# Performance work log

Measured on AMD Instinct MI355X. Metric: run time of the kernel, lower is better.

The kernel has to match this reference:

```python
import jax, jax.numpy as jnp
import numpy as np

B, C, D_MODEL, N_HEADS = 2, 2048, 1024, 16


def rotary_matrix(context_length: int, d: int) -> jnp.ndarray:
    """Faithful vectorization of get_rotary_matrix: theta = 10000^(-2*(i-1)/d)."""
    half = d // 2
    i = jnp.arange(half, dtype=jnp.float32)
    theta = 10000.0 ** (-2.0 * (i - 1.0) / d)          # note the (i-1), as in source
    m = jnp.arange(context_length, dtype=jnp.float32)
    ang = m[:, None] * theta                            # [C, d/2]
    c, s = jnp.cos(ang), jnp.sin(ang)
    ev = 2 * jnp.arange(half)
    od = ev + 1
    R = jnp.zeros((context_length, d, d), jnp.float32)
    R = R.at[:, ev, ev].set(c)
    R = R.at[:, ev, od].set(-s)
    R = R.at[:, od, ev].set(s)
    R = R.at[:, od, od].set(c)
    return R


def setup_inputs() -> dict:
    key = jax.random.key(0)
    k1, k2, k3, k4 = jax.random.split(key, 4)
    x = jax.random.normal(k1, (B, C, D_MODEL), dtype=jnp.float32)
    w_qkv = jax.random.normal(k2, (3 * D_MODEL, D_MODEL), dtype=jnp.float32) * 0.02
    w_out = jax.random.normal(k3, (D_MODEL, D_MODEL), dtype=jnp.float32) * 0.02
    b_out = jax.random.normal(k4, (D_MODEL,), dtype=jnp.float32) * 0.02
    return {"x": x, "w_qkv": w_qkv, "w_out": w_out, "b_out": b_out}


def reference(x, w_qkv, w_out, b_out):
    b, c, d = x.shape
    h = N_HEADS
    dh = d // h
    qkv = x @ w_qkv.T                                   # [B,C,3D]
    q, k, v = jnp.split(qkv, 3, axis=-1)
    # [B,C,D] -> [B,H,C,dh]
    q = q.reshape(b, c, h, dh).transpose(0, 2, 1, 3)
    k = k.reshape(b, c, h, dh).transpose(0, 2, 1, 3)
    v = v.reshape(b, c, h, dh).transpose(0, 2, 1, 3)
    R = rotary_matrix(c, dh)                            # [C,dh,dh]
    q_rot = jnp.einsum('bhci,cij->bhcj', q, R)
    k_rot = jnp.einsum('bhci,cij->bhcj', k, R)
    scale = jnp.sqrt(jnp.float32(dh))
    # exact math of the source: exp with no max subtraction, separate num/den
    attn_num = jnp.exp(jnp.einsum('bhqd,bhkd->bhqk', q_rot, k_rot) / scale)
    attn_den = jnp.exp(jnp.einsum('bhqd,bhkd->bhqk', q, k) / scale)
    attn_den = jnp.sum(attn_den, axis=-1, keepdims=True)
    attn = attn_num / attn_den
    causal = jnp.tril(jnp.ones((c, c), jnp.float32))[None, None]
    attn = jnp.where(causal == 0, 0.0, attn)
    y = jnp.einsum('bhqk,bhkd->bhqd', attn, v)
    y = y.transpose(0, 2, 1, 3).reshape(b, c, d)
    return y @ w_out.T + b_out
```

## Files before the change

kernel.cpp:

```cpp
#include <hip/hip_runtime.h>
#include <math.h>
#include <stdint.h>

#define BB 2
#define CC 2048
#define DD 1024
#define HH 16
#define DHH 64
#define HALF 32

typedef __attribute__((ext_vector_type(8))) short bf16x8;
typedef __attribute__((ext_vector_type(4))) float f32x4;
typedef unsigned int u32;

__device__ __forceinline__ ushort f2bf(float f) {
    uint32_t u = __builtin_bit_cast(uint32_t, f);
    u = (u + 0x7FFFu + ((u >> 16) & 1u)) >> 16;
    return (ushort)u;
}

__device__ __forceinline__ void gload16(const void* g, void* lds) {
    __builtin_amdgcn_global_load_lds(
        (const u32 __attribute__((address_space(1)))*)g,
        (u32 __attribute__((address_space(3)))*)lds, 16, 0, 0);
}

__global__ __launch_bounds__(256) void cast3_k(const float* __restrict__ x,
                                               const float* __restrict__ wq,
                                               const float* __restrict__ wo,
                                               ushort* __restrict__ xb,
                                               ushort* __restrict__ wqb,
                                               ushort* __restrict__ wob) {
    int id = blockIdx.x * 256 + threadIdx.x;
    const float* s;
    ushort* d;
    int off;
    if (id < 524288)       { s = x;  d = xb;  off = id; }
    else if (id < 917504)  { s = wq; d = wqb; off = id - 524288; }
    else                   { s = wo; d = wob; off = id - 917504; }
    float4 a = *reinterpret_cast<const float4*>(s + (size_t)off * 8);
    float4 b = *reinterpret_cast<const float4*>(s + (size_t)off * 8 + 4);
    bf16x8 o;
    o[0] = (short)f2bf(a.x); o[1] = (short)f2bf(a.y);
    o[2] = (short)f2bf(a.z); o[3] = (short)f2bf(a.w);
    o[4] = (short)f2bf(b.x); o[5] = (short)f2bf(b.y);
    o[6] = (short)f2bf(b.z); o[7] = (short)f2bf(b.w);
    *reinterpret_cast<bf16x8*>(d + (size_t)off * 8) = o;
}

__global__ __launch_bounds__(256) void rope_table_k(float* __restrict__ ct, float* __restrict__ st) {
    int idx = blockIdx.x * 256 + threadIdx.x;
    if (idx >= CC * HALF) return;
    int m = idx >> 5;
    int t = idx & 31;
    double theta_d = pow(10000.0, -2.0 * ((double)t - 1.0) / 64.0);
    float theta = (float)theta_d;
    float ang = (float)m * theta;
    ct[idx] = cosf(ang);
    st[idx] = sinf(ang);
}

__global__ __launch_bounds__(256) void qkv_gemm_mfma_k(const ushort* __restrict__ xb,
                                                       const ushort* __restrict__ wqb,
                                                       const float* __restrict__ ct,
                                                       const float* __restrict__ st,
                                                       ushort* __restrict__ q,
                                                       ushort* __restrict__ k,
                                                       ushort* __restrict__ qr,
                                                       ushort* __restrict__ kr,
                                                       ushort* __restrict__ vT3) {
    __shared__ ushort Al[128 * 64];
    __shared__ ushort Bl[128 * 64];
    const int tid = threadIdx.x;
    const int w = tid >> 6, l = tid & 63;
    const int l15 = l & 15, lg = l >> 4;
    const int wr = w >> 1, wc = w & 1;
    const int m0 = blockIdx.x * 128, n0 = blockIdx.y * 128;
    const int lrow = l >> 3, lch = l & 7;

    f32x4 acc[4][4];
#pragma unroll
    for (int i = 0; i < 4; i++)
#pragma unroll
        for (int j = 0; j < 4; j++) acc[i][j] = (f32x4){0.f, 0.f, 0.f, 0.f};

    for (int k0 = 0; k0 < 1024; k0 += 64) {
        __syncthreads();
#pragma unroll
        for (int c = 0; c < 4; c++) {
            int row = w * 32 + c * 8 + lrow;
            int gch = (lch ^ (row & 7)) * 8;
            gload16(xb + (size_t)(m0 + row) * 1024 + k0 + gch, &Al[(w * 32 + c * 8) * 64]);
            gload16(wqb + (size_t)(n0 + row) * 1024 + k0 + gch, &Bl[(w * 32 + c * 8) * 64]);
        }
        __syncthreads();
#pragma unroll
        for (int kk = 0; kk < 2; kk++) {
            bf16x8 a[4], b[4];
#pragma unroll
            for (int mt = 0; mt < 4; mt++) {
                int row = wr * 64 + mt * 16 + l15;
                a[mt] = *reinterpret_cast<const bf16x8*>(&Al[row * 64 + ((kk * 4 + lg) ^ (row & 7)) * 8]);
            }
#pragma unroll
            for (int nt = 0; nt < 4; nt++) {
                int row = wc * 64 + nt * 16 + l15;
                b[nt] = *reinterpret_cast<const bf16x8*>(&Bl[row * 64 + ((kk * 4 + lg) ^ (row & 7)) * 8]);
            }
#pragma unroll
            for (int mt = 0; mt < 4; mt++)
#pragma unroll
                for (int nt = 0; nt < 4; nt++)
                    acc[mt][nt] = __builtin_amdgcn_mfma_f32_16x16x32_bf16(a[mt], b[nt], acc[mt][nt], 0, 0, 0);
        }
    }
#pragma unroll
    for (int mt = 0; mt < 4; mt++)
#pragma unroll
        for (int nt = 0; nt < 4; nt++) {
            int n = n0 + wc * 64 + nt * 16 + l15;
            int part = n >> 10;
            int d = n & 1023;
            int h = d >> 6, dd = d & 63;
            int mbase = m0 + wr * 64 + mt * 16 + lg * 4;
            int bb = mbase >> 11, cpos = mbase & 2047;
            if (part == 2) {
                int kt = cpos >> 6, kcol = cpos & 63;
                ushort4 pk;
                pk.x = f2bf(acc[mt][nt][0]); pk.y = f2bf(acc[mt][nt][1]);
                pk.z = f2bf(acc[mt][nt][2]); pk.w = f2bf(acc[mt][nt][3]);
                size_t off = ((((size_t)(bb * HH + h)) * 32 + kt) * 64 + dd) * 64 + kcol;
                *reinterpret_cast<ushort4*>(vT3 + off) = pk;
            } else {
                ushort* dstu = (part == 0) ? q : k;
                ushort* dstr = (part == 0) ? qr : kr;
                const float sgn = (dd & 1) ? -1.f : 1.f;
                const int t = dd >> 1;
#pragma unroll
                for (int r = 0; r < 4; r++) {
                    float val = acc[mt][nt][r];
                    float par = __shfl_xor(val, 1, 64);
                    float c = ct[(cpos + r) * 32 + t];
                    float s = st[(cpos + r) * 32 + t];
                    float rot = val * c + sgn * par * s;
                    size_t base = (((size_t)bb * HH + h) * CC + (cpos + r)) * DHH + dd;
                    dstu[base] = f2bf(val);
                    dstr[base] = f2bf(rot);
                }
            }
        }
}

__global__ __launch_bounds__(256, 4) void attn_mfma_k(const ushort* __restrict__ qg,
                                                      const ushort* __restrict__ kg,
                                                      const ushort* __restrict__ vT3,
                                                      const ushort* __restrict__ qrg,
                                                      const ushort* __restrict__ krg,
                                                      ushort* __restrict__ y) {
    __shared__ ushort Kl[2][64 * 64];
    __shared__ ushort Krl[2][64 * 64];
    __shared__ ushort Pl[4][16 * 64];

    const int tid = threadIdx.x;
    const int w = tid >> 6, l = tid & 63;
    const int l15 = l & 15, lg = l >> 4;
    const int lrow = l >> 3, lch = l & 7;
    const int bid = blockIdx.x;
    const int bh = bid >> 5;
    const int xt = bid & 31;
    const int tile = (bid & 512) ? (31 - xt) : xt;
    const int q0 = tile * 64;
    const ushort* qb  = qg  + (size_t)bh * CC * DHH;
    const ushort* kb  = kg  + (size_t)bh * CC * DHH;
    const ushort* qrb = qrg + (size_t)bh * CC * DHH;
    const ushort* krb = krg + (size_t)bh * CC * DHH;
    const ushort* vtb = vT3 + (size_t)bh * 32 * 64 * 64;

    bf16x8 qf[2], qrf[2];
#pragma unroll
    for (int kk = 0; kk < 2; kk++) {
        int row = q0 + w * 16 + l15;
        qf[kk]  = *reinterpret_cast<const bf16x8*>(qb  + (size_t)row * DHH + kk * 32 + lg * 8);
        qrf[kk] = *reinterpret_cast<const bf16x8*>(qrb + (size_t)row * DHH + kk * 32 + lg * 8);
    }

    f32x4 yacc[4];
#pragma unroll
    for (int nt = 0; nt < 4; nt++) yacc[nt] = (f32x4){0.f, 0.f, 0.f, 0.f};
    float dacc = 0.f;

#define STAGE(KT, BUF)                                                                        \
    {                                                                                         \
        const int sk0 = (KT) * 64;                                                            \
        const bool sneed = ((KT) <= tile);                                                    \
        _Pragma("unroll")                                                                     \
        for (int c = 0; c < 2; c++) {                                                         \
            int row = w * 16 + c * 8 + lrow;                                                  \
            int gch = (lch ^ (row & 7)) * 8;                                                  \
            gload16(kb + (size_t)(sk0 + row) * DHH + gch, &Kl[BUF][(w * 16 + c * 8) * 64]);   \
            if (sneed)                                                                        \
                gload16(krb + (size_t)(sk0 + row) * DHH + gch, &Krl[BUF][(w * 16 + c * 8) * 64]); \
        }                                                                                     \
    }

    STAGE(0, 0);
    __syncthreads();
    int cur = 0;

    for (int kt = 0; kt < CC / 64; kt++) {
        const bool need = (kt <= tile);

        bf16x8 vf[4][2];
        if (need) {
            const ushort* vt0 = vtb + (size_t)kt * 64 * 64;
#pragma unroll
            for (int nt2 = 0; nt2 < 4; nt2++)
#pragma unroll
                for (int kk2 = 0; kk2 < 2; kk2++)
                    vf[nt2][kk2] = *reinterpret_cast<const bf16x8*>(
                        vt0 + (nt2 * 16 + l15) * 64 + kk2 * 32 + lg * 8);
        }

        if (kt + 1 < CC / 64) STAGE(kt + 1, cur ^ 1);

#pragma unroll
        for (int nt = 0; nt < 4; nt++) {
            f32x4 s = (f32x4){0.f, 0.f, 0.f, 0.f};
#pragma unroll
            for (int kk = 0; kk < 2; kk++) {
                int krow = nt * 16 + l15;
                bf16x8 ka = *reinterpret_cast<const bf16x8*>(
                    &Kl[cur][krow * 64 + ((kk * 4 + lg) ^ (krow & 7)) * 8]);
                s = __builtin_amdgcn_mfma_f32_16x16x32_bf16(ka, qf[kk], s, 0, 0, 0);
            }
#pragma unroll
            for (int r = 0; r < 4; r++)
                dacc += __builtin_amdgcn_exp2f(s[r] * 0.1803368801f);
        }

        if (need) {
            const bool diag = (kt == tile);
            const int qrow = q0 + w * 16 + l15;
#pragma unroll
            for (int nt = 0; nt < 4; nt++) {
                f32x4 s = (f32x4){0.f, 0.f, 0.f, 0.f};
#pragma unroll
                for (int kk = 0; kk < 2; kk++) {
                    int krow = nt * 16 + l15;
                    bf16x8 ka = *reinterpret_cast<const bf16x8*>(
                        &Krl[cur][krow * 64 + ((kk * 4 + lg) ^ (krow & 7)) * 8]);
                    s = __builtin_amdgcn_mfma_f32_16x16x32_bf16(ka, qrf[kk], s, 0, 0, 0);
                }
                float pe[4];
#pragma unroll
                for (int r = 0; r < 4; r++)
                    pe[r] = __builtin_amdgcn_exp2f(s[r] * 0.1803368801f);
                if (diag) {
#pragma unroll
                    for (int r = 0; r < 4; r++) {
                        int key = kt * 64 + nt * 16 + lg * 4 + r;
                        pe[r] = (key <= qrow) ? pe[r] : 0.f;
                    }
                }
                u32 pk0, pk1;
                asm("v_cvt_pk_bf16_f32 %0, %1, %2" : "=v"(pk0) : "v"(pe[0]), "v"(pe[1]));
                asm("v_cvt_pk_bf16_f32 %0, %1, %2" : "=v"(pk1) : "v"(pe[2]), "v"(pe[3]));
                int swzc = (nt * 2 + (lg >> 1)) ^ (l15 & 7);
                uint2 pr; pr.x = pk0; pr.y = pk1;
                *reinterpret_cast<uint2*>(&Pl[w][l15 * 64 + swzc * 8 + (lg & 1) * 4]) = pr;
            }
            bf16x8 pa[2];
#pragma unroll
            for (int kk2 = 0; kk2 < 2; kk2++) {
                int rc = (kk2 * 4 + lg) ^ (l15 & 7);
                pa[kk2] = *reinterpret_cast<const bf16x8*>(&Pl[w][l15 * 64 + rc * 8]);
            }
#pragma unroll
            for (int nt2 = 0; nt2 < 4; nt2++)
#pragma unroll
                for (int kk2 = 0; kk2 < 2; kk2++)
                    yacc[nt2] = __builtin_amdgcn_mfma_f32_16x16x32_bf16(pa[kk2], vf[nt2][kk2],
                                                                        yacc[nt2], 0, 0, 0);
        }
        __syncthreads();
        cur ^= 1;
    }

    float den = dacc;
    den += __shfl_xor(den, 16, 64);
    den += __shfl_xor(den, 32, 64);

    const int b = bh >> 4, h = bh & 15;
#pragma unroll
    for (int r = 0; r < 4; r++) {
        float dr = __shfl(den, lg * 4 + r, 64);
        float inv = 1.f / dr;
        int row = q0 + w * 16 + lg * 4 + r;
#pragma unroll
        for (int nt2 = 0; nt2 < 4; nt2++)
            y[((size_t)b * CC + row) * DD + h * DHH + nt2 * 16 + l15] = f2bf(yacc[nt2][r] * inv);
    }
#undef STAGE
}

__global__ __launch_bounds__(256) void out_proj_mfma_k(const ushort* __restrict__ yb,
                                                       const ushort* __restrict__ wob,
                                                       const float* __restrict__ bias,
                                                       float* __restrict__ out) {
    __shared__ ushort Al[128 * 64];
    __shared__ ushort Bl[128 * 64];
    const int tid = threadIdx.x;
    const int w = tid >> 6, l = tid & 63;
    const int l15 = l & 15, lg = l >> 4;
    const int wr = w >> 1, wc = w & 1;
    const int m0 = blockIdx.x * 128, n0 = blockIdx.y * 128;
    const int lrow = l >> 3, lch = l & 7;

    f32x4 acc[4][4];
#pragma unroll
    for (int i = 0; i < 4; i++)
#pragma unroll
        for (int j = 0; j < 4; j++) acc[i][j] = (f32x4){0.f, 0.f, 0.f, 0.f};

    for (int k0 = 0; k0 < 1024; k0 += 64) {
        __syncthreads();
#pragma unroll
        for (int c = 0; c < 4; c++) {
            int row = w * 32 + c * 8 + lrow;
            int gch = (lch ^ (row & 7)) * 8;
            gload16(yb + (size_t)(m0 + row) * 1024 + k0 + gch, &Al[(w * 32 + c * 8) * 64]);
            gload16(wob + (size_t)(n0 + row) * 1024 + k0 + gch, &Bl[(w * 32 + c * 8) * 64]);
        }
        __syncthreads();
#pragma unroll
        for (int kk = 0; kk < 2; kk++) {
            bf16x8 a[4], b[4];
#pragma unroll
            for (int mt = 0; mt < 4; mt++) {
                int row = wr * 64 + mt * 16 + l15;
                a[mt] = *reinterpret_cast<const bf16x8*>(&Al[row * 64 + ((kk * 4 + lg) ^ (row & 7)) * 8]);
            }
#pragma unroll
            for (int nt = 0; nt < 4; nt++) {
                int row = wc * 64 + nt * 16 + l15;
                b[nt] = *reinterpret_cast<const bf16x8*>(&Bl[row * 64 + ((kk * 4 + lg) ^ (row & 7)) * 8]);
            }
#pragma unroll
            for (int mt = 0; mt < 4; mt++)
#pragma unroll
                for (int nt = 0; nt < 4; nt++)
                    acc[mt][nt] = __builtin_amdgcn_mfma_f32_16x16x32_bf16(a[mt], b[nt], acc[mt][nt], 0, 0, 0);
        }
    }
#pragma unroll
    for (int mt = 0; mt < 4; mt++)
#pragma unroll
        for (int nt = 0; nt < 4; nt++) {
            int n = n0 + wc * 64 + nt * 16 + l15;
            float bv = bias[n];
#pragma unroll
            for (int r = 0; r < 4; r++) {
                int m = m0 + wr * 64 + mt * 16 + lg * 4 + r;
                out[(size_t)m * 1024 + n] = acc[mt][nt][r] + bv;
            }
        }
}

extern "C" void kernel_launch(void* const* d_in, const int* in_sizes, int n_in,
                              void* d_out, int out_size, void* d_ws, size_t ws_size,
                              hipStream_t stream) {
    (void)in_sizes; (void)n_in; (void)out_size; (void)ws_size;
    const float* x     = (const float*)d_in[0];
    const float* w_qkv = (const float*)d_in[1];
    const float* w_out = (const float*)d_in[2];
    const float* b_out = (const float*)d_in[3];
    float* out = (float*)d_out;

    char* p = (char*)d_ws;
    float* ct = (float*)p;  p += (size_t)CC * HALF * 4;
    float* st = (float*)p;  p += (size_t)CC * HALF * 4;
    ushort* xb  = (ushort*)p; p += (size_t)4096 * 1024 * 2;
    ushort* wqb = (ushort*)p; p += (size_t)3072 * 1024 * 2;
    ushort* wob = (ushort*)p; p += (size_t)1024 * 1024 * 2;
    const size_t TEN = (size_t)BB * HH * CC * DHH;
    ushort* qb = (ushort*)p; p += TEN * 2;
    ushort* kb = (ushort*)p; p += TEN * 2;
    ushort* vT = (ushort*)p; p += TEN * 2;
    ushort* qr = (ushort*)p; p += TEN * 2;
    ushort* kr = (ushort*)p; p += TEN * 2;
    ushort* yb = (ushort*)p; p += (size_t)4096 * 1024 * 2;

    cast3_k<<<dim3(4096), dim3(256), 0, stream>>>(x, w_qkv, w_out, xb, wqb, wob);
    rope_table_k<<<dim3((CC * HALF) / 256), dim3(256), 0, stream>>>(ct, st);
    qkv_gemm_mfma_k<<<dim3(32, 24), dim3(256), 0, stream>>>(xb, wqb, ct, st, qb, kb, qr, kr, vT);
    attn_mfma_k<<<dim3(1024), dim3(256), 0, stream>>>(qb, kb, vT, qr, kr, yb);
    out_proj_mfma_k<<<dim3(32, 8), dim3(256), 0, stream>>>(yb, wob, b_out, out);
}
```

Baseline: 172.8 us.

## Load K/Krot/V directly from global in attention, drop LDS staging and barriers

The attention kernel no longer double-buffers K and rotated-K tiles in LDS through async global-to-LDS loads and per-iteration __syncthreads. Each wave now reads K, Krot and V fragments straight from global memory, relying on L2/cache reuse across the four waves. The block index is also remapped so that blocks sharing a batch-head land on the same XCD, and the P scratch uses a padded stride instead of an XOR swizzle. This removes barrier and LDS traffic but gives up software prefetch, so global load latency is exposed inside the MFMA loop and each wave issues its own redundant K reads.

```diff
diff --git a/kernel.cpp b/kernel.cpp
--- a/kernel.cpp
+++ b/kernel.cpp
@@ -151,25 +151,28 @@
         }
 }
 
+#define PSTRIDE 80
 __global__ __launch_bounds__(256, 4) void attn_mfma_k(const ushort* __restrict__ qg,
                                                       const ushort* __restrict__ kg,
                                                       const ushort* __restrict__ vT3,
                                                       const ushort* __restrict__ qrg,
                                                       const ushort* __restrict__ krg,
                                                       ushort* __restrict__ y) {
-    __shared__ ushort Kl[2][64 * 64];
-    __shared__ ushort Krl[2][64 * 64];
-    __shared__ ushort Pl[4][16 * 64];
+    __shared__ ushort Pl[4][16 * PSTRIDE];
 
     const int tid = threadIdx.x;
     const int w = tid >> 6, l = tid & 63;
     const int l15 = l & 15, lg = l >> 4;
-    const int lrow = l >> 3, lch = l & 7;
+
     const int bid = blockIdx.x;
-    const int bh = bid >> 5;
-    const int xt = bid & 31;
-    const int tile = (bid & 512) ? (31 - xt) : xt;
+    const int xcd = bid & 7;
+    const int idx = bid >> 3;
+    const int sub = idx >> 5;
+    const int xt = idx & 31;
+    const int tile = (sub & 1) ? (31 - xt) : xt;
+    const int bh = xcd * 4 + sub;
     const int q0 = tile * 64;
+
     const ushort* qb  = qg  + (size_t)bh * CC * DHH;
     const ushort* kb  = kg  + (size_t)bh * CC * DHH;
     const ushort* qrb = qrg + (size_t)bh * CC * DHH;
@@ -189,48 +192,17 @@
     for (int nt = 0; nt < 4; nt++) yacc[nt] = (f32x4){0.f, 0.f, 0.f, 0.f};
     float dacc = 0.f;
 
-#define STAGE(KT, BUF)                                                                        \
-    {                                                                                         \
-        const int sk0 = (KT) * 64;                                                            \
-        const bool sneed = ((KT) <= tile);                                                    \
-        _Pragma("unroll")                                                                     \
-        for (int c = 0; c < 2; c++) {                                                         \
-            int row = w * 16 + c * 8 + lrow;                                                  \
-            int gch = (lch ^ (row & 7)) * 8;                                                  \
-            gload16(kb + (size_t)(sk0 + row) * DHH + gch, &Kl[BUF][(w * 16 + c * 8) * 64]);   \
-            if (sneed)                                                                        \
-                gload16(krb + (size_t)(sk0 + row) * DHH + gch, &Krl[BUF][(w * 16 + c * 8) * 64]); \
-        }                                                                                     \
-    }
-
-    STAGE(0, 0);
-    __syncthreads();
-    int cur = 0;
-
     for (int kt = 0; kt < CC / 64; kt++) {
+        const int k0 = kt * 64;
         const bool need = (kt <= tile);
-
-        bf16x8 vf[4][2];
-        if (need) {
-            const ushort* vt0 = vtb + (size_t)kt * 64 * 64;
-#pragma unroll
-            for (int nt2 = 0; nt2 < 4; nt2++)
-#pragma unroll
-                for (int kk2 = 0; kk2 < 2; kk2++)
-                    vf[nt2][kk2] = *reinterpret_cast<const bf16x8*>(
-                        vt0 + (nt2 * 16 + l15) * 64 + kk2 * 32 + lg * 8);
-        }
-
-        if (kt + 1 < CC / 64) STAGE(kt + 1, cur ^ 1);
 
 #pragma unroll
         for (int nt = 0; nt < 4; nt++) {
             f32x4 s = (f32x4){0.f, 0.f, 0.f, 0.f};
 #pragma unroll
             for (int kk = 0; kk < 2; kk++) {
-                int krow = nt * 16 + l15;
                 bf16x8 ka = *reinterpret_cast<const bf16x8*>(
-                    &Kl[cur][krow * 64 + ((kk * 4 + lg) ^ (krow & 7)) * 8]);
+                    kb + (size_t)(k0 + nt * 16 + l15) * DHH + kk * 32 + lg * 8);
                 s = __builtin_amdgcn_mfma_f32_16x16x32_bf16(ka, qf[kk], s, 0, 0, 0);
             }
 #pragma unroll
@@ -246,9 +218,8 @@
                 f32x4 s = (f32x4){0.f, 0.f, 0.f, 0.f};
 #pragma unroll
                 for (int kk = 0; kk < 2; kk++) {
-                    int krow = nt * 16 + l15;
                     bf16x8 ka = *reinterpret_cast<const bf16x8*>(
-                        &Krl[cur][krow * 64 + ((kk * 4 + lg) ^ (krow & 7)) * 8]);
+                        krb + (size_t)(k0 + nt * 16 + l15) * DHH + kk * 32 + lg * 8);
                     s = __builtin_amdgcn_mfma_f32_16x16x32_bf16(ka, qrf[kk], s, 0, 0, 0);
                 }
                 float pe[4];
@@ -258,32 +229,30 @@
                 if (diag) {
 #pragma unroll
                     for (int r = 0; r < 4; r++) {
-                        int key = kt * 64 + nt * 16 + lg * 4 + r;
+                        int key = k0 + nt * 16 + lg * 4 + r;
                         pe[r] = (key <= qrow) ? pe[r] : 0.f;
                     }
                 }
                 u32 pk0, pk1;
                 asm("v_cvt_pk_bf16_f32 %0, %1, %2" : "=v"(pk0) : "v"(pe[0]), "v"(pe[1]));
                 asm("v_cvt_pk_bf16_f32 %0, %1, %2" : "=v"(pk1) : "v"(pe[2]), "v"(pe[3]));
-                int swzc = (nt * 2 + (lg >> 1)) ^ (l15 & 7);
                 uint2 pr; pr.x = pk0; pr.y = pk1;
-                *reinterpret_cast<uint2*>(&Pl[w][l15 * 64 + swzc * 8 + (lg & 1) * 4]) = pr;
+                *reinterpret_cast<uint2*>(&Pl[w][l15 * PSTRIDE + nt * 16 + lg * 4]) = pr;
             }
             bf16x8 pa[2];
 #pragma unroll
-            for (int kk2 = 0; kk2 < 2; kk2++) {
-                int rc = (kk2 * 4 + lg) ^ (l15 & 7);
-                pa[kk2] = *reinterpret_cast<const bf16x8*>(&Pl[w][l15 * 64 + rc * 8]);
-            }
+            for (int kk2 = 0; kk2 < 2; kk2++)
+                pa[kk2] = *reinterpret_cast<const bf16x8*>(&Pl[w][l15 * PSTRIDE + kk2 * 32 + lg * 8]);
+            const ushort* vt0 = vtb + (size_t)kt * 64 * 64;
 #pragma unroll
             for (int nt2 = 0; nt2 < 4; nt2++)
 #pragma unroll
-                for (int kk2 = 0; kk2 < 2; kk2++)
-                    yacc[nt2] = __builtin_amdgcn_mfma_f32_16x16x32_bf16(pa[kk2], vf[nt2][kk2],
-                                                                        yacc[nt2], 0, 0, 0);
-        }
-        __syncthreads();
-        cur ^= 1;
+                for (int kk2 = 0; kk2 < 2; kk2++) {
+                    bf16x8 bv = *reinterpret_cast<const bf16x8*>(
+                        vt0 + (nt2 * 16 + l15) * 64 + kk2 * 32 + lg * 8);
+                    yacc[nt2] = __builtin_amdgcn_mfma_f32_16x16x32_bf16(pa[kk2], bv, yacc[nt2], 0, 0, 0);
+                }
+        }
     }
 
     float den = dacc;
@@ -300,7 +269,6 @@
         for (int nt2 = 0; nt2 < 4; nt2++)
             y[((size_t)b * CC + row) * DD + h * DHH + nt2 * 16 + l15] = f2bf(yacc[nt2][r] * inv);
     }
-#undef STAGE
 }
 
 __global__ __launch_bounds__(256) void out_proj_mfma_k(const ushort* __restrict__ yb,
```

Result: slower. 310.4 us (+79.7%).

## Split non-causal denominator into separate kernel and trim attention loop to causal tiles

Applied to the files above, without the earlier changes.

The full-row softmax denominator, which needs every key, moves out of the attention kernel into a new den_k kernel that tiles 128 queries by 128 keys and writes per-row sums to workspace. The attention kernel now loops only over causal key tiles, loads only rotated K, and reads the precomputed denominator at the end. Blocks are remapped so each XCD works on a fixed subset of heads, and occupancy is raised to 5 blocks per SIMD. The aim is to remove the per-tile load imbalance where every block walked all 32 key tiles. The cost is an extra kernel launch and a second pass over Q and K.

```diff
diff --git a/kernel.cpp b/kernel.cpp
--- a/kernel.cpp
+++ b/kernel.cpp
@@ -12,6 +12,8 @@
 typedef __attribute__((ext_vector_type(8))) short bf16x8;
 typedef __attribute__((ext_vector_type(4))) float f32x4;
 typedef unsigned int u32;
+
+#define EXPC 0.1803368801f
 
 __device__ __forceinline__ ushort f2bf(float f) {
     uint32_t u = __builtin_bit_cast(uint32_t, f);
@@ -151,78 +153,146 @@
         }
 }
 
-__global__ __launch_bounds__(256, 4) void attn_mfma_k(const ushort* __restrict__ qg,
-                                                      const ushort* __restrict__ kg,
-                                                      const ushort* __restrict__ vT3,
-                                                      const ushort* __restrict__ qrg,
-                                                      const ushort* __restrict__ krg,
-                                                      ushort* __restrict__ y) {
-    __shared__ ushort Kl[2][64 * 64];
-    __shared__ ushort Krl[2][64 * 64];
-    __shared__ ushort Pl[4][16 * 64];
-
+__global__ __launch_bounds__(256) void den_k(const ushort* __restrict__ qg,
+                                             const ushort* __restrict__ kg,
+                                             float* __restrict__ deng) {
+    __shared__ ushort Kd[2][128 * 64];
     const int tid = threadIdx.x;
     const int w = tid >> 6, l = tid & 63;
     const int l15 = l & 15, lg = l >> 4;
     const int lrow = l >> 3, lch = l & 7;
+    const int bh = blockIdx.y;
+    const int q0 = blockIdx.x * 128;
+    const ushort* qb = qg + (size_t)bh * CC * DHH;
+    const ushort* kb = kg + (size_t)bh * CC * DHH;
+
+    bf16x8 qf[2][2];
+#pragma unroll
+    for (int mt = 0; mt < 2; mt++)
+#pragma unroll
+        for (int kk = 0; kk < 2; kk++) {
+            int row = q0 + w * 32 + mt * 16 + l15;
+            qf[mt][kk] = *reinterpret_cast<const bf16x8*>(qb + (size_t)row * DHH + kk * 32 + lg * 8);
+        }
+
+    float dacc[2] = {0.f, 0.f};
+
+#define DSTAGE(KT, BUF)                                                                     \
+    {                                                                                       \
+        const int sk0 = (KT) * 128;                                                         \
+        _Pragma("unroll")                                                                   \
+        for (int c = 0; c < 4; c++) {                                                       \
+            int row = w * 32 + c * 8 + lrow;                                                \
+            int gch = (lch ^ (row & 7)) * 8;                                                \
+            gload16(kb + (size_t)(sk0 + row) * DHH + gch, &Kd[BUF][(w * 32 + c * 8) * 64]); \
+        }                                                                                   \
+    }
+
+    DSTAGE(0, 0);
+    __syncthreads();
+    int cur = 0;
+
+    for (int kt = 0; kt < 16; kt++) {
+        if (kt < 15) DSTAGE(kt + 1, cur ^ 1);
+#pragma unroll
+        for (int nt = 0; nt < 8; nt++) {
+            bf16x8 ka[2];
+#pragma unroll
+            for (int kk = 0; kk < 2; kk++) {
+                int krow = nt * 16 + l15;
+                ka[kk] = *reinterpret_cast<const bf16x8*>(
+                    &Kd[cur][krow * 64 + ((kk * 4 + lg) ^ (krow & 7)) * 8]);
+            }
+#pragma unroll
+            for (int mt = 0; mt < 2; mt++) {
+                f32x4 s = (f32x4){0.f, 0.f, 0.f, 0.f};
+                s = __builtin_amdgcn_mfma_f32_16x16x32_bf16(ka[0], qf[mt][0], s, 0, 0, 0);
+                s = __builtin_amdgcn_mfma_f32_16x16x32_bf16(ka[1], qf[mt][1], s, 0, 0, 0);
+#pragma unroll
+                for (int r = 0; r < 4; r++)
+                    dacc[mt] += __builtin_amdgcn_exp2f(s[r] * EXPC);
+            }
+        }
+        __syncthreads();
+        cur ^= 1;
+    }
+#pragma unroll
+    for (int mt = 0; mt < 2; mt++) {
+        float d = dacc[mt];
+        d += __shfl_xor(d, 16, 64);
+        d += __shfl_xor(d, 32, 64);
+        if (lg == 0)
+            deng[(size_t)bh * CC + q0 + w * 32 + mt * 16 + l15] = d;
+    }
+#undef DSTAGE
+}
+
+__global__ __launch_bounds__(256, 5) void attn_mfma_k(const ushort* __restrict__ vT3,
+                                                      const ushort* __restrict__ qrg,
+                                                      const ushort* __restrict__ krg,
+                                                      const float* __restrict__ deng,
+                                                      ushort* __restrict__ y) {
+    __shared__ ushort Krl[2][64 * 64];
+    __shared__ ushort Pl[4][16 * 64];
+
+    const int tid = threadIdx.x;
+    const int w = tid >> 6, l = tid & 63;
+    const int l15 = l & 15, lg = l >> 4;
+    const int lrow = l >> 3, lch = l & 7;
+
     const int bid = blockIdx.x;
-    const int bh = bid >> 5;
-    const int xt = bid & 31;
-    const int tile = (bid & 512) ? (31 - xt) : xt;
+    const int xcd = bid & 7;
+    const int idx = bid >> 3;
+    const int sub = idx >> 5;
+    const int xt = idx & 31;
+    const int tile = (sub & 1) ? (31 - xt) : xt;
+    const int bh = xcd * 4 + sub;
     const int q0 = tile * 64;
-    const ushort* qb  = qg  + (size_t)bh * CC * DHH;
-    const ushort* kb  = kg  + (size_t)bh * CC * DHH;
+
     const ushort* qrb = qrg + (size_t)bh * CC * DHH;
     const ushort* krb = krg + (size_t)bh * CC * DHH;
     const ushort* vtb = vT3 + (size_t)bh * 32 * 64 * 64;
 
-    bf16x8 qf[2], qrf[2];
+    bf16x8 qrf[2];
 #pragma unroll
     for (int kk = 0; kk < 2; kk++) {
         int row = q0 + w * 16 + l15;
-        qf[kk]  = *reinterpret_cast<const bf16x8*>(qb  + (size_t)row * DHH + kk * 32 + lg * 8);
         qrf[kk] = *reinterpret_cast<const bf16x8*>(qrb + (size_t)row * DHH + kk * 32 + lg * 8);
     }
 
     f32x4 yacc[4];
 #pragma unroll
     for (int nt = 0; nt < 4; nt++) yacc[nt] = (f32x4){0.f, 0.f, 0.f, 0.f};
-    float dacc = 0.f;
-
-#define STAGE(KT, BUF)                                                                        \
-    {                                                                                         \
-        const int sk0 = (KT) * 64;                                                            \
-        const bool sneed = ((KT) <= tile);                                                    \
-        _Pragma("unroll")                                                                     \
-        for (int c = 0; c < 2; c++) {                                                         \
-            int row = w * 16 + c * 8 + lrow;                                                  \
-            int gch = (lch ^ (row & 7)) * 8;                                                  \
-            gload16(kb + (size_t)(sk0 + row) * DHH + gch, &Kl[BUF][(w * 16 + c * 8) * 64]);   \
-            if (sneed)                                                                        \
-                gload16(krb + (size_t)(sk0 + row) * DHH + gch, &Krl[BUF][(w * 16 + c * 8) * 64]); \
-        }                                                                                     \
+
+#define STAGE(KT, BUF)                                                                         \
+    {                                                                                          \
+        const int sk0 = (KT) * 64;                                                             \
+        _Pragma("unroll")                                                                      \
+        for (int c = 0; c < 2; c++) {                                                          \
+            int row = w * 16 + c * 8 + lrow;                                                   \
+            int gch = (lch ^ (row & 7)) * 8;                                                   \
+            gload16(krb + (size_t)(sk0 + row) * DHH + gch, &Krl[BUF][(w * 16 + c * 8) * 64]);  \
+        }                                                                                      \
     }
 
     STAGE(0, 0);
     __syncthreads();
     int cur = 0;
 
-    for (int kt = 0; kt < CC / 64; kt++) {
-        const bool need = (kt <= tile);
-
+    for (int kt = 0; kt <= tile; kt++) {
         bf16x8 vf[4][2];
-        if (need) {
-            const ushort* vt0 = vtb + (size_t)kt * 64 * 64;
-#pragma unroll
-            for (int nt2 = 0; nt2 < 4; nt2++)
-#pragma unroll
-                for (int kk2 = 0; kk2 < 2; kk2++)
-                    vf[nt2][kk2] = *reinterpret_cast<const bf16x8*>(
-                        vt0 + (nt2 * 16 + l15) * 64 + kk2 * 32 + lg * 8);
-        }
-
-        if (kt + 1 < CC / 64) STAGE(kt + 1, cur ^ 1);
-
+        const ushort* vt0 = vtb + (size_t)kt * 64 * 64;
+#pragma unroll
+        for (int nt2 = 0; nt2 < 4; nt2++)
+#pragma unroll
+            for (int kk2 = 0; kk2 < 2; kk2++)
+                vf[nt2][kk2] = *reinterpret_cast<const bf16x8*>(
+                    vt0 + (nt2 * 16 + l15) * 64 + kk2 * 32 + lg * 8);
+
+        if (kt < tile) STAGE(kt + 1, cur ^ 1);
+
+        const bool diag = (kt == tile);
+        const int qrow = q0 + w * 16 + l15;
 #pragma unroll
         for (int nt = 0; nt < 4; nt++) {
             f32x4 s = (f32x4){0.f, 0.f, 0.f, 0.f};
@@ -230,72 +300,48 @@
             for (int kk = 0; kk < 2; kk++) {
                 int krow = nt * 16 + l15;
                 bf16x8 ka = *reinterpret_cast<const bf16x8*>(
-                    &Kl[cur][krow * 64 + ((kk * 4 + lg) ^ (krow & 7)) * 8]);
-                s = __builtin_amdgcn_mfma_f32_16x16x32_bf16(ka, qf[kk], s, 0, 0, 0);
-            }
+                    &Krl[cur][krow * 64 + ((kk * 4 + lg) ^ (krow & 7)) * 8]);
+                s = __builtin_amdgcn_mfma_f32_16x16x32_bf16(ka, qrf[kk], s, 0, 0, 0);
+            }
+            float pe[4];
 #pragma unroll
             for (int r = 0; r < 4; r++)
-                dacc += __builtin_amdgcn_exp2f(s[r] * 0.1803368801f);
-        }
-
-        if (need) {
-            const bool diag = (kt == tile);
-            const int qrow = q0 + w * 16 + l15;
-#pragma unroll
-            for (int nt = 0; nt < 4; nt++) {
-                f32x4 s = (f32x4){0.f, 0.f, 0.f, 0.f};
-#pragma unroll
-                for (int kk = 0; kk < 2; kk++) {
-                    int krow = nt * 16 + l15;
-                    bf16x8 ka = *reinterpret_cast<const bf16x8*>(
-                        &Krl[cur][krow * 64 + ((kk * 4 + lg) ^ (krow & 7)) * 8]);
-                    s = __builtin_amdgcn_mfma_f32_16x16x32_bf16(ka, qrf[kk], s, 0, 0, 0);
+                pe[r] = __builtin_amdgcn_exp2f(s[r] * EXPC);
+            if (diag) {
+#pragma unroll
+                for (int r = 0; r < 4; r++) {
+                    int key = kt * 64 + nt * 16 + lg * 4 + r;
+                    pe[r] = (key <= qrow) ? pe[r] : 0.f;
                 }
-                float pe[4];
-#pragma unroll
-                for (int r = 0; r < 4; r++)
-                    pe[r] = __builtin_amdgcn_exp2f(s[r] * 0.1803368801f);
-                if (diag) {
-#pragma unroll
-                    for (int r = 0; r < 4; r++) {
-                        int key = kt * 64 + nt * 16 + lg * 4 + r;
-                        pe[r] = (key <= qrow) ? pe[r] : 0.f;
-                    }
-                }
-                u32 pk0, pk1;
-                asm("v_cvt_pk_bf16_f32 %0, %1, %2" : "=v"(pk0) : "v"(pe[0]), "v"(pe[1]));
-                asm("v_cvt_pk_bf16_f32 %0, %1, %2" : "=v"(pk1) : "v"(pe[2]), "v"(pe[3]));
-                int swzc = (nt * 2 + (lg >> 1)) ^ (l15 & 7);
-                uint2 pr; pr.x = pk0; pr.y = pk1;
-                *reinterpret_cast<uint2*>(&Pl[w][l15 * 64 + swzc * 8 + (lg & 1) * 4]) = pr;
-            }
-            bf16x8 pa[2];
-#pragma unroll
-            for (int kk2 = 0; kk2 < 2; kk2++) {
-                int rc = (kk2 * 4 + lg) ^ (l15 & 7);
-                pa[kk2] = *reinterpret_cast<const bf16x8*>(&Pl[w][l15 * 64 + rc * 8]);
-            }
-#pragma unroll
-            for (int nt2 = 0; nt2 < 4; nt2++)
-#pragma unroll
-                for (int kk2 = 0; kk2 < 2; kk2++)
-                    yacc[nt2] = __builtin_amdgcn_mfma_f32_16x16x32_bf16(pa[kk2], vf[nt2][kk2],
-                                                                        yacc[nt2], 0, 0, 0);
-        }
+            }
+            u32 pk0, pk1;
+            asm("v_cvt_pk_bf16_f32 %0, %1, %2" : "=v"(pk0) : "v"(pe[0]), "v"(pe[1]));
+            asm("v_cvt_pk_bf16_f32 %0, %1, %2" : "=v"(pk1) : "v"(pe[2]), "v"(pe[3]));
+            int swzc = (nt * 2 + (lg >> 1)) ^ (l15 & 7);
+            uint2 pr; pr.x = pk0; pr.y = pk1;
+            *reinterpret_cast<uint2*>(&Pl[w][l15 * 64 + swzc * 8 + (lg & 1) * 4]) = pr;
+        }
+        bf16x8 pa[2];
+#pragma unroll
+        for (int kk2 = 0; kk2 < 2; kk2++) {
+            int rc = (kk2 * 4 + lg) ^ (l15 & 7);
+            pa[kk2] = *reinterpret_cast<const bf16x8*>(&Pl[w][l15 * 64 + rc * 8]);
+        }
+#pragma unroll
+        for (int nt2 = 0; nt2 < 4; nt2++)
+#pragma unroll
+            for (int kk2 = 0; kk2 < 2; kk2++)
+                yacc[nt2] = __builtin_amdgcn_mfma_f32_16x16x32_bf16(pa[kk2], vf[nt2][kk2],
+                                                                    yacc[nt2], 0, 0, 0);
         __syncthreads();
         cur ^= 1;
     }
 
-    float den = dacc;
-    den += __shfl_xor(den, 16, 64);
-    den += __shfl_xor(den, 32, 64);
-
     const int b = bh >> 4, h = bh & 15;
 #pragma unroll
     for (int r = 0; r < 4; r++) {
-        float dr = __shfl(den, lg * 4 + r, 64);
-        float inv = 1.f / dr;
         int row = q0 + w * 16 + lg * 4 + r;
+        float inv = 1.f / deng[(size_t)bh * CC + row];
 #pragma unroll
         for (int nt2 = 0; nt2 < 4; nt2++)
             y[((size_t)b * CC + row) * DD + h * DHH + nt2 * 16 + l15] = f2bf(yacc[nt2][r] * inv);
@@ -389,10 +435,12 @@
     ushort* qr = (ushort*)p; p += TEN * 2;
     ushort* kr = (ushort*)p; p += TEN * 2;
     ushort* yb = (ushort*)p; p += (size_t)4096 * 1024 * 2;
+    float* den = (float*)p;  p += (size_t)32 * CC * 4;
 
     cast3_k<<<dim3(4096), dim3(256), 0, stream>>>(x, w_qkv, w_out, xb, wqb, wob);
     rope_table_k<<<dim3((CC * HALF) / 256), dim3(256), 0, stream>>>(ct, st);
     qkv_gemm_mfma_k<<<dim3(32, 24), dim3(256), 0, stream>>>(xb, wqb, ct, st, qb, kb, qr, kr, vT);
-    attn_mfma_k<<<dim3(1024), dim3(256), 0, stream>>>(qb, kb, vT, qr, kr, yb);
+    den_k<<<dim3(16, 32), dim3(256), 0, stream>>>(qb, kb, den);
+    attn_mfma_k<<<dim3(1024), dim3(256), 0, stream>>>(vT, qr, kr, den, yb);
     out_proj_mfma_k<<<dim3(32, 8), dim3(256), 0, stream>>>(yb, wob, b_out, out);
 }
```

After: 181.0 us. 4.8% more time.

## Pair causal query tiles per block, XCD-aware mapping, MFMA priority hints

Applied to the files above, without the earlier changes.

Each block now handles half of a short causal tile (waves 0-1) and half of its mirror long tile (waves 2-3), so every block gets balanced work and reuses one staged K/Kr stream for both tiles. Block indices are remapped so that all blocks for a given batch-head land on the same XCD, which should improve L2 reuse of K/V. The change also raises MFMA issue priority with s_setprio, splits the denominator accumulator into two chains, and lowers the launch-bounds occupancy hint from 4 to 2 blocks per CU. In exchange, waves inside a block diverge in trip count and the short-tile waves sit idle at barriers, and the lower occupancy hint may let the compiler use more registers.

```diff
diff --git a/kernel.cpp b/kernel.cpp
--- a/kernel.cpp
+++ b/kernel.cpp
@@ -12,6 +12,8 @@
 typedef __attribute__((ext_vector_type(8))) short bf16x8;
 typedef __attribute__((ext_vector_type(4))) float f32x4;
 typedef unsigned int u32;
+
+#define EXPC 0.1803368801f
 
 __device__ __forceinline__ ushort f2bf(float f) {
     uint32_t u = __builtin_bit_cast(uint32_t, f);
@@ -151,12 +153,12 @@
         }
 }
 
-__global__ __launch_bounds__(256, 4) void attn_mfma_k(const ushort* __restrict__ qg,
-                                                      const ushort* __restrict__ kg,
-                                                      const ushort* __restrict__ vT3,
-                                                      const ushort* __restrict__ qrg,
-                                                      const ushort* __restrict__ krg,
-                                                      ushort* __restrict__ y) {
+__global__ __launch_bounds__(256, 2) void attn_fused_k(const ushort* __restrict__ vT3,
+                                                       const ushort* __restrict__ qg,
+                                                       const ushort* __restrict__ kg,
+                                                       const ushort* __restrict__ qrg,
+                                                       const ushort* __restrict__ krg,
+                                                       ushort* __restrict__ y) {
     __shared__ ushort Kl[2][64 * 64];
     __shared__ ushort Krl[2][64 * 64];
     __shared__ ushort Pl[4][16 * 64];
@@ -165,11 +167,20 @@
     const int w = tid >> 6, l = tid & 63;
     const int l15 = l & 15, lg = l >> 4;
     const int lrow = l >> 3, lch = l & 7;
+
     const int bid = blockIdx.x;
-    const int bh = bid >> 5;
-    const int xt = bid & 31;
-    const int tile = (bid & 512) ? (31 - xt) : xt;
-    const int q0 = tile * 64;
+    const int xcd = bid & 7;
+    const int idx = bid >> 3;
+    const int sub = idx & 3;
+    const int rest = idx >> 2;
+    const int tp = rest >> 1;
+    const int rh = rest & 1;
+    const int bh = xcd * 4 + sub;
+    const int NB = 31 - tp;
+    const int myTile = (w < 2) ? tp : NB;
+    const int myLast = myTile;
+    const int qrow0 = myTile * 64 + rh * 32 + (w & 1) * 16;
+
     const ushort* qb  = qg  + (size_t)bh * CC * DHH;
     const ushort* kb  = kg  + (size_t)bh * CC * DHH;
     const ushort* qrb = qrg + (size_t)bh * CC * DHH;
@@ -179,39 +190,37 @@
     bf16x8 qf[2], qrf[2];
 #pragma unroll
     for (int kk = 0; kk < 2; kk++) {
-        int row = q0 + w * 16 + l15;
-        qf[kk]  = *reinterpret_cast<const bf16x8*>(qb  + (size_t)row * DHH + kk * 32 + lg * 8);
-        qrf[kk] = *reinterpret_cast<const bf16x8*>(qrb + (size_t)row * DHH + kk * 32 + lg * 8);
+        qf[kk]  = *reinterpret_cast<const bf16x8*>(qb  + (size_t)(qrow0 + l15) * DHH + kk * 32 + lg * 8);
+        qrf[kk] = *reinterpret_cast<const bf16x8*>(qrb + (size_t)(qrow0 + l15) * DHH + kk * 32 + lg * 8);
     }
 
     f32x4 yacc[4];
 #pragma unroll
     for (int nt = 0; nt < 4; nt++) yacc[nt] = (f32x4){0.f, 0.f, 0.f, 0.f};
-    float dacc = 0.f;
-
-#define STAGE(KT, BUF)                                                                        \
-    {                                                                                         \
-        const int sk0 = (KT) * 64;                                                            \
-        const bool sneed = ((KT) <= tile);                                                    \
-        _Pragma("unroll")                                                                     \
-        for (int c = 0; c < 2; c++) {                                                         \
-            int row = w * 16 + c * 8 + lrow;                                                  \
-            int gch = (lch ^ (row & 7)) * 8;                                                  \
-            gload16(kb + (size_t)(sk0 + row) * DHH + gch, &Kl[BUF][(w * 16 + c * 8) * 64]);   \
-            if (sneed)                                                                        \
+    float dacc0 = 0.f, dacc1 = 0.f;
+
+#define STAGE(KT, BUF)                                                                         \
+    {                                                                                          \
+        const int sk0 = (KT) * 64;                                                             \
+        _Pragma("unroll")                                                                      \
+        for (int c = 0; c < 2; c++) {                                                          \
+            int row = w * 16 + c * 8 + lrow;                                                   \
+            int gch = (lch ^ (row & 7)) * 8;                                                   \
+            gload16(kb + (size_t)(sk0 + row) * DHH + gch, &Kl[BUF][(w * 16 + c * 8) * 64]);    \
+            if ((KT) <= NB)                                                                    \
                 gload16(krb + (size_t)(sk0 + row) * DHH + gch, &Krl[BUF][(w * 16 + c * 8) * 64]); \
-        }                                                                                     \
+        }                                                                                      \
     }
 
     STAGE(0, 0);
     __syncthreads();
     int cur = 0;
 
-    for (int kt = 0; kt < CC / 64; kt++) {
-        const bool need = (kt <= tile);
+    for (int kt = 0; kt < 32; kt++) {
+        const bool active = (kt <= myLast);
 
         bf16x8 vf[4][2];
-        if (need) {
+        if (active) {
             const ushort* vt0 = vtb + (size_t)kt * 64 * 64;
 #pragma unroll
             for (int nt2 = 0; nt2 < 4; nt2++)
@@ -221,40 +230,50 @@
                         vt0 + (nt2 * 16 + l15) * 64 + kk2 * 32 + lg * 8);
         }
 
-        if (kt + 1 < CC / 64) STAGE(kt + 1, cur ^ 1);
+        if (kt + 1 < 32) STAGE(kt + 1, cur ^ 1);
 
 #pragma unroll
         for (int nt = 0; nt < 4; nt++) {
+            bf16x8 ka0, ka1;
+            {
+                int krow = nt * 16 + l15;
+                ka0 = *reinterpret_cast<const bf16x8*>(&Kl[cur][krow * 64 + ((0 + lg) ^ (krow & 7)) * 8]);
+                ka1 = *reinterpret_cast<const bf16x8*>(&Kl[cur][krow * 64 + ((4 + lg) ^ (krow & 7)) * 8]);
+            }
+            __builtin_amdgcn_s_setprio(1);
             f32x4 s = (f32x4){0.f, 0.f, 0.f, 0.f};
-#pragma unroll
-            for (int kk = 0; kk < 2; kk++) {
-                int krow = nt * 16 + l15;
-                bf16x8 ka = *reinterpret_cast<const bf16x8*>(
-                    &Kl[cur][krow * 64 + ((kk * 4 + lg) ^ (krow & 7)) * 8]);
-                s = __builtin_amdgcn_mfma_f32_16x16x32_bf16(ka, qf[kk], s, 0, 0, 0);
-            }
-#pragma unroll
-            for (int r = 0; r < 4; r++)
-                dacc += __builtin_amdgcn_exp2f(s[r] * 0.1803368801f);
-        }
-
-        if (need) {
-            const bool diag = (kt == tile);
-            const int qrow = q0 + w * 16 + l15;
+            s = __builtin_amdgcn_mfma_f32_16x16x32_bf16(ka0, qf[0], s, 0, 0, 0);
+            s = __builtin_amdgcn_mfma_f32_16x16x32_bf16(ka1, qf[1], s, 0, 0, 0);
+            __builtin_amdgcn_s_setprio(0);
+            if (nt & 1) {
+#pragma unroll
+                for (int r = 0; r < 4; r++) dacc1 += __builtin_amdgcn_exp2f(s[r] * EXPC);
+            } else {
+#pragma unroll
+                for (int r = 0; r < 4; r++) dacc0 += __builtin_amdgcn_exp2f(s[r] * EXPC);
+            }
+        }
+
+        if (active) {
+            const bool diag = (kt == myLast);
+            const int qrow = qrow0 + l15;
 #pragma unroll
             for (int nt = 0; nt < 4; nt++) {
+                bf16x8 kra0, kra1;
+                {
+                    int krow = nt * 16 + l15;
+                    kra0 = *reinterpret_cast<const bf16x8*>(&Krl[cur][krow * 64 + ((0 + lg) ^ (krow & 7)) * 8]);
+                    kra1 = *reinterpret_cast<const bf16x8*>(&Krl[cur][krow * 64 + ((4 + lg) ^ (krow & 7)) * 8]);
+                }
+                __builtin_amdgcn_s_setprio(1);
                 f32x4 s = (f32x4){0.f, 0.f, 0.f, 0.f};
-#pragma unroll
-                for (int kk = 0; kk < 2; kk++) {
-                    int krow = nt * 16 + l15;
-                    bf16x8 ka = *reinterpret_cast<const bf16x8*>(
-                        &Krl[cur][krow * 64 + ((kk * 4 + lg) ^ (krow & 7)) * 8]);
-                    s = __builtin_amdgcn_mfma_f32_16x16x32_bf16(ka, qrf[kk], s, 0, 0, 0);
-                }
+                s = __builtin_amdgcn_mfma_f32_16x16x32_bf16(kra0, qrf[0], s, 0, 0, 0);
+                s = __builtin_amdgcn_mfma_f32_16x16x32_bf16(kra1, qrf[1], s, 0, 0, 0);
+                __builtin_amdgcn_s_setprio(0);
                 float pe[4];
 #pragma unroll
                 for (int r = 0; r < 4; r++)
-                    pe[r] = __builtin_amdgcn_exp2f(s[r] * 0.1803368801f);
+                    pe[r] = __builtin_amdgcn_exp2f(s[r] * EXPC);
                 if (diag) {
 #pragma unroll
                     for (int r = 0; r < 4; r++) {
@@ -275,18 +294,20 @@
                 int rc = (kk2 * 4 + lg) ^ (l15 & 7);
                 pa[kk2] = *reinterpret_cast<const bf16x8*>(&Pl[w][l15 * 64 + rc * 8]);
             }
-#pragma unroll
-            for (int nt2 = 0; nt2 < 4; nt2++)
-#pragma unroll
-                for (int kk2 = 0; kk2 < 2; kk2++)
-                    yacc[nt2] = __builtin_amdgcn_mfma_f32_16x16x32_bf16(pa[kk2], vf[nt2][kk2],
-                                                                        yacc[nt2], 0, 0, 0);
-        }
+            __builtin_amdgcn_s_setprio(1);
+#pragma unroll
+            for (int nt2 = 0; nt2 < 4; nt2++) {
+                yacc[nt2] = __builtin_amdgcn_mfma_f32_16x16x32_bf16(pa[0], vf[nt2][0], yacc[nt2], 0, 0, 0);
+                yacc[nt2] = __builtin_amdgcn_mfma_f32_16x16x32_bf16(pa[1], vf[nt2][1], yacc[nt2], 0, 0, 0);
+            }
+            __builtin_amdgcn_s_setprio(0);
+        }
+
         __syncthreads();
         cur ^= 1;
     }
 
-    float den = dacc;
+    float den = dacc0 + dacc1;
     den += __shfl_xor(den, 16, 64);
     den += __shfl_xor(den, 32, 64);
 
@@ -295,7 +316,7 @@
     for (int r = 0; r < 4; r++) {
         float dr = __shfl(den, lg * 4 + r, 64);
         float inv = 1.f / dr;
-        int row = q0 + w * 16 + lg * 4 + r;
+        int row = qrow0 + lg * 4 + r;
 #pragma unroll
         for (int nt2 = 0; nt2 < 4; nt2++)
             y[((size_t)b * CC + row) * DD + h * DHH + nt2 * 16 + l15] = f2bf(yacc[nt2][r] * inv);
@@ -393,6 +414,6 @@
     cast3_k<<<dim3(4096), dim3(256), 0, stream>>>(x, w_qkv, w_out, xb, wqb, wob);
     rope_table_k<<<dim3((CC * HALF) / 256), dim3(256), 0, stream>>>(ct, st);
     qkv_gemm_mfma_k<<<dim3(32, 24), dim3(256), 0, stream>>>(xb, wqb, ct, st, qb, kb, qr, kr, vT);
-    attn_mfma_k<<<dim3(1024), dim3(256), 0, stream>>>(qb, kb, vT, qr, kr, yb);
+    attn_fused_k<<<dim3(1024), dim3(256), 0, stream>>>(vT, qb, kb, qr, kr, yb);
     out_proj_mfma_k<<<dim3(32, 8), dim3(256), 0, stream>>>(yb, wob, b_out, out);
 }
```

Result: no change. 171.4 us (-0.8%).
